# Kernel optimization log

Hardware: AMD Instinct MI355X
Metric: run time of the kernel (lower is better)

The kernel has to match this reference:

```python
import jax, jax.numpy as jnp
import numpy as np
import math

B, N, DIM = 2, 4096, 1024
H, D, M = 16, 64, 256


def setup_inputs() -> dict:
    key = jax.random.key(0)
    ks = jax.random.split(key, 6)
    s = 1.0 / math.sqrt(DIM)
    return {
        "x": jax.random.normal(ks[0], (B, N, DIM), dtype=jnp.float32),
        "w_q": jax.random.normal(ks[1], (DIM, H * D), dtype=jnp.float32) * s,
        "w_k": jax.random.normal(ks[2], (DIM, H * D), dtype=jnp.float32) * s,
        "w_v": jax.random.normal(ks[3], (DIM, H * D), dtype=jnp.float32) * s,
        "w_o": jax.random.normal(ks[4], (H * D, DIM), dtype=jnp.float32) * s,
        "b_o": jnp.zeros((DIM,), dtype=jnp.float32),
        "omega": jax.random.normal(ks[5], (M, D), dtype=jnp.float32),
    }


def _heads(t):
    # [B, N, H*D] -> [B, H, N, D]
    return t.reshape(B, N, H, D).transpose(0, 2, 1, 3)


def _phi(t, omega):
    # t: [B,H,N,D], omega: [M,D] -> [B,H,N,M]
    proj = jnp.einsum("bhnd,md->bhnm", t, omega)
    norm = 0.5 * jnp.sum(t * t, axis=-1, keepdims=True)
    return jnp.exp(proj - norm) / math.sqrt(M)


def reference(x, w_q, w_k, w_v, w_o, b_o, omega):
    q = _heads(x @ w_q)
    k = _heads(x @ w_k)
    v = _heads(x @ w_v)
    phi_q = _phi(q, omega)          # [B,H,N,M]
    phi_k = _phi(k, omega)          # [B,H,N,M]
    kv = jnp.einsum("bhnm,bhnd->bhmd", phi_k, v)   # [B,H,M,D]
    k_sum = phi_k.sum(axis=2)                       # [B,H,M]
    z = 1.0 / (jnp.einsum("bhnm,bhm->bhn", phi_q, k_sum) + 1e-6)
    out = jnp.einsum("bhnm,bhmd->bhnd", phi_q, kv) * z[..., None]
    out = out.transpose(0, 2, 1, 3).reshape(B, N, H * D)
    return out @ w_o + b_o
```

## Files before the change

### kernel.cpp

```cpp
#include <hip/hip_runtime.h>

#define DEVI __device__ __forceinline__

using f32x4 = __attribute__((ext_vector_type(4))) float;
using fvec4 = __attribute__((ext_vector_type(4))) float;
using s16x4 = __attribute__((ext_vector_type(4))) short;
using s16x8 = __attribute__((ext_vector_type(8))) short;

DEVI unsigned short f2bf_rn(float f) {
  union { float f; unsigned u; } v; v.f = f;
  unsigned r = v.u + 0x7fffu + ((v.u >> 16) & 1u);
  return (unsigned short)(r >> 16);
}
DEVI float bf2f(unsigned short h) {
  union { unsigned u; float f; } v; v.u = ((unsigned)h) << 16;
  return v.f;
}
DEVI f32x4 mfma16(s16x8 a, s16x8 b, f32x4 c) {
  return __builtin_amdgcn_mfma_f32_16x16x32_bf16(a, b, c, 0, 0, 0);
}
DEVI void gld16(const void* g, void* lds) {
  __builtin_amdgcn_global_load_lds(
      (const __attribute__((address_space(1))) unsigned int*)g,
      (__attribute__((address_space(3))) unsigned int*)lds, 16, 0, 0);
}

__global__ __launch_bounds__(256) void k_split_x(
    const float* __restrict__ X,
    unsigned short* __restrict__ XH, unsigned short* __restrict__ XL)
{
  size_t i = ((size_t)blockIdx.x * 256 + threadIdx.x) * 8;
  fvec4 a = *(const fvec4*)&X[i];
  fvec4 b = *(const fvec4*)&X[i + 4];
  s16x8 hv, lv;
#pragma unroll
  for (int j = 0; j < 4; ++j) {
    unsigned short h = f2bf_rn(a[j]);
    hv[j] = (short)h; lv[j] = (short)f2bf_rn(a[j] - bf2f(h));
  }
#pragma unroll
  for (int j = 0; j < 4; ++j) {
    unsigned short h = f2bf_rn(b[j]);
    hv[4 + j] = (short)h; lv[4 + j] = (short)f2bf_rn(b[j] - bf2f(h));
  }
  *(s16x8*)&XH[i] = hv;
  *(s16x8*)&XL[i] = lv;
}

__global__ __launch_bounds__(256) void k_prep_w(
    const float* __restrict__ wq, const float* __restrict__ wk,
    const float* __restrict__ wv, const float* __restrict__ wo,
    unsigned short* __restrict__ WTh, unsigned short* __restrict__ WOT)
{
  __shared__ float tile[64][65];
  const int z = blockIdx.z;
  const float* src = (z == 0) ? wq : (z == 1) ? wk : (z == 2) ? wv : wo;
  const int k0 = blockIdx.x * 64;
  const int n0 = blockIdx.y * 64;
  const int t = threadIdx.x;
#pragma unroll
  for (int j = 0; j < 4; ++j) {
    int r = (t >> 4) + 16 * j;
    int c = (t & 15) * 4;
    fvec4 v = *(const fvec4*)&src[(size_t)(k0 + r) * 1024 + n0 + c];
#pragma unroll
    for (int i = 0; i < 4; ++i) tile[r][c + i] = v[i];
  }
  __syncthreads();
#pragma unroll
  for (int j = 0; j < 4; ++j) {
    int n = (t >> 4) + 16 * j;
    int kc = (t & 15) * 4;
    s16x4 hv;
#pragma unroll
    for (int i = 0; i < 4; ++i) hv[i] = (short)f2bf_rn(tile[kc + i][n]);
    if (z < 3) {
      *(s16x4*)&WTh[(size_t)(z * 1024 + n0 + n) * 1024 + k0 + kc] = hv;
    } else {
      *(s16x4*)&WOT[(size_t)(n0 + n) * 1024 + k0 + kc] = hv;
    }
  }
}

__global__ __launch_bounds__(256) void k_gemm_qkv(
    const unsigned short* __restrict__ XH, const unsigned short* __restrict__ XL,
    const unsigned short* __restrict__ WTh,
    unsigned short* __restrict__ QH, unsigned short* __restrict__ QL,
    unsigned short* __restrict__ KH, unsigned short* __restrict__ KL,
    unsigned short* __restrict__ VB)
{
  __shared__ unsigned short AH[128 * 32], AL[128 * 32], BH[128 * 32];
  const int cb = blockIdx.x;
  const int rb = blockIdx.y;
  const int t = threadIdx.x;
  const int w = t >> 6, l = t & 63;
  const bool tp = (cb < 16);
  f32x4 acc[4][4];
#pragma unroll
  for (int a = 0; a < 4; ++a)
#pragma unroll
    for (int b = 0; b < 4; ++b) acc[a][b] = (f32x4)0.f;

  const int r0 = w * 32;
  const int lrow = l >> 2;
  const int lcol = (l & 3) * 8;
  const size_t gA0 = (size_t)(rb * 128 + r0 + lrow) * 1024 + lcol;
  const size_t gA1 = gA0 + (size_t)16 * 1024;
  const size_t gB0 = (size_t)(cb * 128 + r0 + lrow) * 1024 + lcol;
  const size_t gB1 = gB0 + (size_t)16 * 1024;
  unsigned short* ldsA0 = &AH[r0 * 32];
  unsigned short* ldsA1 = &AH[(r0 + 16) * 32];
  unsigned short* ldsL0 = &AL[r0 * 32];
  unsigned short* ldsL1 = &AL[(r0 + 16) * 32];
  unsigned short* ldsB0 = &BH[r0 * 32];
  unsigned short* ldsB1 = &BH[(r0 + 16) * 32];

  const int wm = (w & 1) * 64, wn = (w >> 1) * 64;
  const int lr = l & 15, ko = (l >> 4) * 8;

  for (int ks = 0; ks < 32; ++ks) {
    const int k0 = ks * 32;
    gld16(&XH[gA0 + k0], ldsA0);
    gld16(&XH[gA1 + k0], ldsA1);
    if (tp) {
      gld16(&XL[gA0 + k0], ldsL0);
      gld16(&XL[gA1 + k0], ldsL1);
    }
    gld16(&WTh[gB0 + k0], ldsB0);
    gld16(&WTh[gB1 + k0], ldsB1);
    __syncthreads();
    s16x8 ah[4], al[4], bh[4];
#pragma unroll
    for (int f = 0; f < 4; ++f) {
      ah[f] = *(const s16x8*)&AH[(wm + f * 16 + lr) * 32 + ko];
      bh[f] = *(const s16x8*)&BH[(wn + f * 16 + lr) * 32 + ko];
    }
    if (tp) {
#pragma unroll
      for (int f = 0; f < 4; ++f) al[f] = *(const s16x8*)&AL[(wm + f * 16 + lr) * 32 + ko];
    }
#pragma unroll
    for (int fa = 0; fa < 4; ++fa)
#pragma unroll
      for (int fb = 0; fb < 4; ++fb) {
        acc[fa][fb] = mfma16(ah[fa], bh[fb], acc[fa][fb]);
        if (tp) acc[fa][fb] = mfma16(al[fa], bh[fb], acc[fa][fb]);
      }
    __syncthreads();
  }
  const int lg = l >> 4;
#pragma unroll
  for (int fa = 0; fa < 4; ++fa)
#pragma unroll
    for (int r = 0; r < 4; ++r) {
      int row = rb * 128 + wm + fa * 16 + lg * 4 + r;
#pragma unroll
      for (int fb = 0; fb < 4; ++fb) {
        int col = cb * 128 + wn + fb * 16 + lr;
        float v = acc[fa][fb][r];
        unsigned short hs = f2bf_rn(v);
        if (cb < 8) {
          QH[(size_t)row * 1024 + col] = hs;
          QL[(size_t)row * 1024 + col] = f2bf_rn(v - bf2f(hs));
        } else if (cb < 16) {
          KH[(size_t)row * 1024 + col - 1024] = hs;
          KL[(size_t)row * 1024 + col - 1024] = f2bf_rn(v - bf2f(hs));
        } else {
          VB[(size_t)row * 1024 + col - 2048] = hs;
        }
      }
    }
}

__global__ __launch_bounds__(512, 1) void k_phik_kv(
    const unsigned short* __restrict__ KH, const unsigned short* __restrict__ KL,
    const unsigned short* __restrict__ VB,
    const float* __restrict__ omega, float* __restrict__ KVP)
{
  __shared__ unsigned short OH[256][72];
  __shared__ unsigned short KHs[64][72], KLs[64][72];
  __shared__ unsigned short PKT[256][72];
  __shared__ unsigned short AVT[80][72];
  __shared__ float norm_s[64];
  const int nc = blockIdx.x;
  const int bh = blockIdx.y;
  const int b = bh >> 4, h = bh & 15;
  const int t = threadIdx.x, w = t >> 6, l = t & 63;
  const int lr = l & 15, lg = l >> 4, ko8 = lg * 8;

#pragma unroll
  for (int j = 0; j < 8; ++j) {
    int e = j * 512 + t;
    int m = e >> 4, c = (e & 15) * 4;
    fvec4 v = *(const fvec4*)&omega[m * 64 + c];
    s16x4 hv;
#pragma unroll
    for (int i = 0; i < 4; ++i) hv[i] = (short)f2bf_rn(v[i]);
    *(s16x4*)&OH[m][c] = hv;
  }
  for (int e = t; e < 16 * 64; e += 512) {
    int rr = e >> 6, cc = e & 63;
    AVT[64 + rr][cc] = (rr == 0) ? (unsigned short)0x3F80 : (unsigned short)0;
  }

  f32x4 acc2[5][2];
#pragma unroll
  for (int a = 0; a < 5; ++a)
#pragma unroll
    for (int bb = 0; bb < 2; ++bb) acc2[a][bb] = (f32x4)0.f;

  for (int st = 0; st < 8; ++st) {
    const int n0 = nc * 512 + st * 64;
    __syncthreads();
    {
      int r = t >> 3, c8 = (t & 7) * 8;
      size_t o = (size_t)(b * 4096 + n0 + r) * 1024 + h * 64 + c8;
      s16x8 vh = *(const s16x8*)&KH[o];
      s16x8 vl = *(const s16x8*)&KL[o];
      *(s16x8*)&KHs[r][c8] = vh;
      *(s16x8*)&KLs[r][c8] = vl;
      float ss = 0.f;
#pragma unroll
      for (int i = 0; i < 8; ++i) {
        float q = bf2f((unsigned short)vh[i]) + bf2f((unsigned short)vl[i]);
        ss += q * q;
      }
      ss += __shfl_xor(ss, 1);
      ss += __shfl_xor(ss, 2);
      ss += __shfl_xor(ss, 4);
      if ((t & 7) == 0) norm_s[r] = 0.5f * ss;
    }
    {
      int n = t >> 3, dq = (t & 7) * 8;
      s16x8 v = *(const s16x8*)&VB[(size_t)(b * 4096 + n0 + n) * 1024 + h * 64 + dq];
#pragma unroll
      for (int i = 0; i < 8; ++i) AVT[dq + i][n] = (unsigned short)v[i];
    }
    __syncthreads();
    f32x4 acc[4][2];
#pragma unroll
    for (int a = 0; a < 4; ++a)
#pragma unroll
      for (int bb = 0; bb < 2; ++bb) acc[a][bb] = (f32x4)0.f;
#pragma unroll
    for (int ksub = 0; ksub < 2; ++ksub) {
      int ko = ksub * 32 + ko8;
      s16x8 ah[4], al[4], bh[2];
#pragma unroll
      for (int f = 0; f < 4; ++f) {
        ah[f] = *(const s16x8*)&KHs[f * 16 + lr][ko];
        al[f] = *(const s16x8*)&KLs[f * 16 + lr][ko];
      }
#pragma unroll
      for (int f = 0; f < 2; ++f) bh[f] = *(const s16x8*)&OH[w * 32 + f * 16 + lr][ko];
#pragma unroll
      for (int fa = 0; fa < 4; ++fa)
#pragma unroll
        for (int fb = 0; fb < 2; ++fb) {
          acc[fa][fb] = mfma16(ah[fa], bh[fb], acc[fa][fb]);
          acc[fa][fb] = mfma16(al[fa], bh[fb], acc[fa][fb]);
        }
    }
#pragma unroll
    for (int fa = 0; fa < 4; ++fa)
#pragma unroll
      for (int r = 0; r < 4; ++r) {
        int n = fa * 16 + lg * 4 + r;
        float nm = norm_s[n];
#pragma unroll
        for (int fb = 0; fb < 2; ++fb) {
          int m = w * 32 + fb * 16 + lr;
          float p = __expf(acc[fa][fb][r] - nm) * 0.0625f;
          PKT[m][n] = f2bf_rn(p);
        }
      }
    __syncthreads();
#pragma unroll
    for (int ksub = 0; ksub < 2; ++ksub) {
      int ko = ksub * 32 + ko8;
      s16x8 fA[5], fB[2];
#pragma unroll
      for (int f = 0; f < 5; ++f) fA[f] = *(const s16x8*)&AVT[f * 16 + lr][ko];
#pragma unroll
      for (int f = 0; f < 2; ++f) fB[f] = *(const s16x8*)&PKT[w * 32 + f * 16 + lr][ko];
#pragma unroll
      for (int fa = 0; fa < 5; ++fa)
#pragma unroll
        for (int fb = 0; fb < 2; ++fb) acc2[fa][fb] = mfma16(fA[fa], fB[fb], acc2[fa][fb]);
    }
  }
#pragma unroll
  for (int fa = 0; fa < 5; ++fa)
#pragma unroll
    for (int r = 0; r < 4; ++r) {
      int dp = fa * 16 + lg * 4 + r;
#pragma unroll
      for (int fb = 0; fb < 2; ++fb) {
        int m = w * 32 + fb * 16 + lr;
        KVP[(size_t)((bh * 8 + nc) * 80 + dp) * 256 + m] = acc2[fa][fb][r];
      }
    }
}

__global__ __launch_bounds__(256) void k_kv_reduce(
    const float* __restrict__ KVP, float* __restrict__ KVT)
{
  int idx = blockIdx.x * 256 + threadIdx.x;
  if (idx >= 32 * 80 * 256) return;
  int bh = idx / (80 * 256);
  int rem = idx % (80 * 256);
  float s = 0.f;
#pragma unroll
  for (int nci = 0; nci < 8; ++nci) s += KVP[(size_t)(bh * 8 + nci) * 80 * 256 + rem];
  KVT[idx] = s;
}

__global__ __launch_bounds__(256) void k_phiq_attn(
    const unsigned short* QH, const unsigned short* QL,
    const float* __restrict__ omega, const float* __restrict__ KVT,
    unsigned short* ATT)
{
  __shared__ unsigned short QHs[64][72], QLs[64][72];
  __shared__ unsigned short OH[256][72];
  __shared__ unsigned short PQ[64][264];
  __shared__ unsigned short KVB[80][264];
  __shared__ float norm_s[64];
  const int nt = blockIdx.x;
  const int bh = blockIdx.y;
  const int t = threadIdx.x, w = t >> 6, l = t & 63;
  const int b = bh >> 4, h = bh & 15;
  const int lr = l & 15, lg = l >> 4, ko8 = lg * 8;

  {
    int r = t >> 2, cq = (t & 3) * 4;
    float ss = 0.f;
#pragma unroll
    for (int j = 0; j < 4; ++j) {
      int c = cq + 16 * j;
      size_t o = (size_t)(b * 4096 + nt * 64 + r) * 1024 + h * 64 + c;
      s16x4 vh = *(const s16x4*)&QH[o];
      s16x4 vl = *(const s16x4*)&QL[o];
      *(s16x4*)&QHs[r][c] = vh;
      *(s16x4*)&QLs[r][c] = vl;
#pragma unroll
      for (int i = 0; i < 4; ++i) {
        float q = bf2f((unsigned short)vh[i]) + bf2f((unsigned short)vl[i]);
        ss += q * q;
      }
    }
    ss += __shfl_xor(ss, 1);
    ss += __shfl_xor(ss, 2);
    if ((t & 3) == 0) norm_s[r] = 0.5f * ss;
  }
#pragma unroll
  for (int j = 0; j < 16; ++j) {
    int e = j * 256 + t;
    int m = e >> 4, c = (e & 15) * 4;
    fvec4 v = *(const fvec4*)&omega[m * 64 + c];
    s16x4 hv;
#pragma unroll
    for (int i = 0; i < 4; ++i) hv[i] = (short)f2bf_rn(v[i]);
    *(s16x4*)&OH[m][c] = hv;
  }
#pragma unroll
  for (int j = 0; j < 20; ++j) {
    int e = (j * 256 + t) * 4;
    int dp = e >> 8, m = e & 255;
    fvec4 v = *(const fvec4*)&KVT[(size_t)bh * 80 * 256 + dp * 256 + m];
    s16x4 hv;
#pragma unroll
    for (int i = 0; i < 4; ++i) hv[i] = (short)f2bf_rn(v[i]);
    *(s16x4*)&KVB[dp][m] = hv;
  }
  __syncthreads();
  f32x4 acc[4][4];
#pragma unroll
  for (int a = 0; a < 4; ++a)
#pragma unroll
    for (int bb = 0; bb < 4; ++bb) acc[a][bb] = (f32x4)0.f;
#pragma unroll
  for (int ksub = 0; ksub < 2; ++ksub) {
    int ko = ksub * 32 + ko8;
    s16x8 ah[4], al[4], bh[4];
#pragma unroll
    for (int f = 0; f < 4; ++f) {
      ah[f] = *(const s16x8*)&QHs[f * 16 + lr][ko];
      al[f] = *(const s16x8*)&QLs[f * 16 + lr][ko];
      bh[f] = *(const s16x8*)&OH[w * 64 + f * 16 + lr][ko];
    }
#pragma unroll
    for (int fa = 0; fa < 4; ++fa)
#pragma unroll
      for (int fb = 0; fb < 4; ++fb) {
        acc[fa][fb] = mfma16(ah[fa], bh[fb], acc[fa][fb]);
        acc[fa][fb] = mfma16(al[fa], bh[fb], acc[fa][fb]);
      }
  }
#pragma unroll
  for (int fa = 0; fa < 4; ++fa)
#pragma unroll
    for (int r = 0; r < 4; ++r) {
      int n = fa * 16 + lg * 4 + r;
      float nm = norm_s[n];
#pragma unroll
      for (int fb = 0; fb < 4; ++fb) {
        int m = w * 64 + fb * 16 + lr;
        float p = __expf(acc[fa][fb][r] - nm) * 0.0625f;
        PQ[n][m] = f2bf_rn(p);
      }
    }
  __syncthreads();
  f32x4 acc2[5];
#pragma unroll
  for (int bb = 0; bb < 5; ++bb) acc2[bb] = (f32x4)0.f;
  for (int ks = 0; ks < 8; ++ks) {
    const int m0 = ks * 32;
    s16x8 fA = *(const s16x8*)&PQ[w * 16 + lr][m0 + ko8];
    s16x8 fB[5];
#pragma unroll
    for (int f = 0; f < 5; ++f) fB[f] = *(const s16x8*)&KVB[f * 16 + lr][m0 + ko8];
#pragma unroll
    for (int fb = 0; fb < 5; ++fb) acc2[fb] = mfma16(fA, fB[fb], acc2[fb]);
  }
#pragma unroll
  for (int r = 0; r < 4; ++r) {
    float den = __shfl(acc2[4][r], (l & 48));
    float z = 1.f / (den + 1e-6f);
    int n = nt * 64 + w * 16 + lg * 4 + r;
#pragma unroll
    for (int fb = 0; fb < 4; ++fb) {
      int col = h * 64 + fb * 16 + lr;
      ATT[(size_t)(b * 4096 + n) * 1024 + col] = f2bf_rn(acc2[fb][r] * z);
    }
  }
}

__global__ __launch_bounds__(256) void k_gemm_out(
    const unsigned short* __restrict__ ATT,
    const unsigned short* __restrict__ WOT,
    const float* __restrict__ b_o,
    float* __restrict__ OUT)
{
  __shared__ unsigned short As[128 * 32], Bs[128 * 32];
  const int cb = blockIdx.x;
  const int rb = blockIdx.y;
  const int t = threadIdx.x, w = t >> 6, l = t & 63;
  f32x4 acc[4][4];
#pragma unroll
  for (int a = 0; a < 4; ++a)
#pragma unroll
    for (int bb = 0; bb < 4; ++bb) acc[a][bb] = (f32x4)0.f;

  const int r0 = w * 32;
  const int lrow = l >> 2;
  const int lcol = (l & 3) * 8;
  const size_t gA0 = (size_t)(rb * 128 + r0 + lrow) * 1024 + lcol;
  const size_t gA1 = gA0 + (size_t)16 * 1024;
  const size_t gB0 = (size_t)(cb * 128 + r0 + lrow) * 1024 + lcol;
  const size_t gB1 = gB0 + (size_t)16 * 1024;
  unsigned short* ldsA0 = &As[r0 * 32];
  unsigned short* ldsA1 = &As[(r0 + 16) * 32];
  unsigned short* ldsB0 = &Bs[r0 * 32];
  unsigned short* ldsB1 = &Bs[(r0 + 16) * 32];

  const int wm = (w & 1) * 64, wn = (w >> 1) * 64;
  const int lr = l & 15, ko = (l >> 4) * 8;

  for (int ks = 0; ks < 32; ++ks) {
    const int k0 = ks * 32;
    gld16(&ATT[gA0 + k0], ldsA0);
    gld16(&ATT[gA1 + k0], ldsA1);
    gld16(&WOT[gB0 + k0], ldsB0);
    gld16(&WOT[gB1 + k0], ldsB1);
    __syncthreads();
    s16x8 fA[4], fB[4];
#pragma unroll
    for (int f = 0; f < 4; ++f) {
      fA[f] = *(const s16x8*)&As[(wm + f * 16 + lr) * 32 + ko];
      fB[f] = *(const s16x8*)&Bs[(wn + f * 16 + lr) * 32 + ko];
    }
#pragma unroll
    for (int fa = 0; fa < 4; ++fa)
#pragma unroll
      for (int fb = 0; fb < 4; ++fb) acc[fa][fb] = mfma16(fA[fa], fB[fb], acc[fa][fb]);
    __syncthreads();
  }
  const int lg = l >> 4;
#pragma unroll
  for (int fa = 0; fa < 4; ++fa)
#pragma unroll
    for (int r = 0; r < 4; ++r) {
      int row = rb * 128 + wm + fa * 16 + lg * 4 + r;
#pragma unroll
      for (int fb = 0; fb < 4; ++fb) {
        int col = cb * 128 + wn + fb * 16 + lr;
        OUT[(size_t)row * 1024 + col] = acc[fa][fb][r] + b_o[col];
      }
    }
}

extern "C" void kernel_launch(void* const* d_in, const int* in_sizes, int n_in,
                              void* d_out, int out_size, void* d_ws, size_t ws_size,
                              hipStream_t stream)
{
  const float* x  = (const float*)d_in[0];
  const float* wq = (const float*)d_in[1];
  const float* wk = (const float*)d_in[2];
  const float* wv = (const float*)d_in[3];
  const float* wo = (const float*)d_in[4];
  const float* bo = (const float*)d_in[5];
  const float* om = (const float*)d_in[6];
  float* out = (float*)d_out;

  const size_t PLANE = (size_t)8192 * 1024 * 2;
  char* ws = (char*)d_ws;
  unsigned short* WOT = (unsigned short*)(ws);
  char* segB = ws + 2097152;
  char* segC = segB + 2 * PLANE;
  char* segD = segC + 4 * PLANE;
  char* segE = segD + 26214400;

  unsigned short* QH  = (unsigned short*)segB;
  unsigned short* QL  = (unsigned short*)(segB + PLANE);
  unsigned short* ATT = (unsigned short*)segB;

  unsigned short* KH  = (unsigned short*)segC;
  unsigned short* KL  = (unsigned short*)(segC + PLANE);
  unsigned short* VB  = (unsigned short*)(segC + 2 * PLANE);
  unsigned short* XH  = (unsigned short*)(segC + 3 * PLANE);

  unsigned short* WTh = (unsigned short*)segD;
  unsigned short* XL  = (unsigned short*)(segD + 6291456);
  float* KVP = (float*)segD;
  float* KVT = (float*)segE;

  k_split_x<<<dim3(4096), 256, 0, stream>>>(x, XH, XL);
  k_prep_w<<<dim3(16, 16, 4), 256, 0, stream>>>(wq, wk, wv, wo, WTh, WOT);
  k_gemm_qkv<<<dim3(24, 64), 256, 0, stream>>>(XH, XL, WTh, QH, QL, KH, KL, VB);
  k_phik_kv<<<dim3(8, 32), 512, 0, stream>>>(KH, KL, VB, om, KVP);
  k_kv_reduce<<<dim3(2560), 256, 0, stream>>>(KVP, KVT);
  k_phiq_attn<<<dim3(64, 32), 256, 0, stream>>>(QH, QL, om, KVT, ATT);
  k_gemm_out<<<dim3(8, 64), 256, 0, stream>>>(ATT, WOT, bo, out);
}
```

Measured before the change: 233.3 us.

## Double-buffer LDS in QKV and output GEMMs and split QKV by precision

Both GEMM kernels now use two LDS buffers and prefetch the next K-slice with global_load_lds before computing the current one. Explicit vmcnt waits and raw barriers replace the two __syncthreads per iteration. The QKV GEMM becomes a template on whether the low-precision X plane is used, launched as two kernels (Q/K with hi+lo, V with hi only), which removes the per-block runtime branch and sizes LDS per variant. The cost is double the LDS footprint, which may lower occupancy, plus an extra kernel launch. The hand-counted vmcnt values must match the number of issued loads.

```diff
diff --git a/kernel.cpp b/kernel.cpp
--- a/kernel.cpp
+++ b/kernel.cpp
@@ -82,19 +82,21 @@
   }
 }
 
-__global__ __launch_bounds__(256) void k_gemm_qkv(
+template <bool TP>
+__global__ __launch_bounds__(256) void k_gemm_qkv_t(
     const unsigned short* __restrict__ XH, const unsigned short* __restrict__ XL,
-    const unsigned short* __restrict__ WTh,
+    const unsigned short* __restrict__ WTh, int cb_base,
     unsigned short* __restrict__ QH, unsigned short* __restrict__ QL,
     unsigned short* __restrict__ KH, unsigned short* __restrict__ KL,
     unsigned short* __restrict__ VB)
 {
-  __shared__ unsigned short AH[128 * 32], AL[128 * 32], BH[128 * 32];
-  const int cb = blockIdx.x;
+  __shared__ unsigned short AH[2][128 * 32];
+  __shared__ unsigned short BHs[2][128 * 32];
+  __shared__ unsigned short AL[TP ? 2 : 1][128 * 32];
+  const int cb = cb_base + blockIdx.x;
   const int rb = blockIdx.y;
   const int t = threadIdx.x;
   const int w = t >> 6, l = t & 63;
-  const bool tp = (cb < 16);
   f32x4 acc[4][4];
 #pragma unroll
   for (int a = 0; a < 4; ++a)
@@ -104,49 +106,58 @@
   const int r0 = w * 32;
   const int lrow = l >> 2;
   const int lcol = (l & 3) * 8;
-  const size_t gA0 = (size_t)(rb * 128 + r0 + lrow) * 1024 + lcol;
-  const size_t gA1 = gA0 + (size_t)16 * 1024;
-  const size_t gB0 = (size_t)(cb * 128 + r0 + lrow) * 1024 + lcol;
-  const size_t gB1 = gB0 + (size_t)16 * 1024;
-  unsigned short* ldsA0 = &AH[r0 * 32];
-  unsigned short* ldsA1 = &AH[(r0 + 16) * 32];
-  unsigned short* ldsL0 = &AL[r0 * 32];
-  unsigned short* ldsL1 = &AL[(r0 + 16) * 32];
-  unsigned short* ldsB0 = &BH[r0 * 32];
-  unsigned short* ldsB1 = &BH[(r0 + 16) * 32];
+  const size_t gA = (size_t)(rb * 128 + r0 + lrow) * 1024 + lcol;
+  const size_t gB = (size_t)(cb * 128 + r0 + lrow) * 1024 + lcol;
+  const int lds0 = r0 * 32;
+  const int lds1 = (r0 + 16) * 32;
 
   const int wm = (w & 1) * 64, wn = (w >> 1) * 64;
   const int lr = l & 15, ko = (l >> 4) * 8;
 
+  auto STAGE = [&](int buf, int k0) {
+    gld16(&XH[gA + k0], &AH[buf][lds0]);
+    gld16(&XH[gA + (size_t)16 * 1024 + k0], &AH[buf][lds1]);
+    if constexpr (TP) {
+      gld16(&XL[gA + k0], &AL[buf][lds0]);
+      gld16(&XL[gA + (size_t)16 * 1024 + k0], &AL[buf][lds1]);
+    }
+    gld16(&WTh[gB + k0], &BHs[buf][lds0]);
+    gld16(&WTh[gB + (size_t)16 * 1024 + k0], &BHs[buf][lds1]);
+  };
+
+  STAGE(0, 0);
+  int cur = 0;
   for (int ks = 0; ks < 32; ++ks) {
-    const int k0 = ks * 32;
-    gld16(&XH[gA0 + k0], ldsA0);
-    gld16(&XH[gA1 + k0], ldsA1);
-    if (tp) {
-      gld16(&XL[gA0 + k0], ldsL0);
-      gld16(&XL[gA1 + k0], ldsL1);
-    }
-    gld16(&WTh[gB0 + k0], ldsB0);
-    gld16(&WTh[gB1 + k0], ldsB1);
-    __syncthreads();
+    if (ks < 31) {
+      STAGE(cur ^ 1, (ks + 1) * 32);
+      if constexpr (TP) asm volatile("s_waitcnt vmcnt(6)" ::: "memory");
+      else              asm volatile("s_waitcnt vmcnt(4)" ::: "memory");
+    } else {
+      asm volatile("s_waitcnt vmcnt(0)" ::: "memory");
+    }
+    __builtin_amdgcn_s_barrier();
+    asm volatile("" ::: "memory");
     s16x8 ah[4], al[4], bh[4];
 #pragma unroll
     for (int f = 0; f < 4; ++f) {
-      ah[f] = *(const s16x8*)&AH[(wm + f * 16 + lr) * 32 + ko];
-      bh[f] = *(const s16x8*)&BH[(wn + f * 16 + lr) * 32 + ko];
-    }
-    if (tp) {
-#pragma unroll
-      for (int f = 0; f < 4; ++f) al[f] = *(const s16x8*)&AL[(wm + f * 16 + lr) * 32 + ko];
+      ah[f] = *(const s16x8*)&AH[cur][(wm + f * 16 + lr) * 32 + ko];
+      bh[f] = *(const s16x8*)&BHs[cur][(wn + f * 16 + lr) * 32 + ko];
+    }
+    if constexpr (TP) {
+#pragma unroll
+      for (int f = 0; f < 4; ++f) al[f] = *(const s16x8*)&AL[cur][(wm + f * 16 + lr) * 32 + ko];
     }
 #pragma unroll
     for (int fa = 0; fa < 4; ++fa)
 #pragma unroll
       for (int fb = 0; fb < 4; ++fb) {
         acc[fa][fb] = mfma16(ah[fa], bh[fb], acc[fa][fb]);
-        if (tp) acc[fa][fb] = mfma16(al[fa], bh[fb], acc[fa][fb]);
-      }
-    __syncthreads();
+        if constexpr (TP) acc[fa][fb] = mfma16(al[fa], bh[fb], acc[fa][fb]);
+      }
+    asm volatile("s_waitcnt lgkmcnt(0)" ::: "memory");
+    __builtin_amdgcn_s_barrier();
+    asm volatile("" ::: "memory");
+    cur ^= 1;
   }
   const int lg = l >> 4;
 #pragma unroll
@@ -158,15 +169,18 @@
       for (int fb = 0; fb < 4; ++fb) {
         int col = cb * 128 + wn + fb * 16 + lr;
         float v = acc[fa][fb][r];
-        unsigned short hs = f2bf_rn(v);
-        if (cb < 8) {
-          QH[(size_t)row * 1024 + col] = hs;
-          QL[(size_t)row * 1024 + col] = f2bf_rn(v - bf2f(hs));
-        } else if (cb < 16) {
-          KH[(size_t)row * 1024 + col - 1024] = hs;
-          KL[(size_t)row * 1024 + col - 1024] = f2bf_rn(v - bf2f(hs));
+        if constexpr (TP) {
+          unsigned short hs = f2bf_rn(v);
+          unsigned short ls = f2bf_rn(v - bf2f(hs));
+          if (cb < 8) {
+            QH[(size_t)row * 1024 + col] = hs;
+            QL[(size_t)row * 1024 + col] = ls;
+          } else {
+            KH[(size_t)row * 1024 + col - 1024] = hs;
+            KL[(size_t)row * 1024 + col - 1024] = ls;
+          }
         } else {
-          VB[(size_t)row * 1024 + col - 2048] = hs;
+          VB[(size_t)row * 1024 + col - 2048] = f2bf_rn(v);
         }
       }
     }
@@ -441,7 +455,7 @@
     const float* __restrict__ b_o,
     float* __restrict__ OUT)
 {
-  __shared__ unsigned short As[128 * 32], Bs[128 * 32];
+  __shared__ unsigned short As[2][128 * 32], Bs[2][128 * 32];
   const int cb = blockIdx.x;
   const int rb = blockIdx.y;
   const int t = threadIdx.x, w = t >> 6, l = t & 63;
@@ -454,36 +468,46 @@
   const int r0 = w * 32;
   const int lrow = l >> 2;
   const int lcol = (l & 3) * 8;
-  const size_t gA0 = (size_t)(rb * 128 + r0 + lrow) * 1024 + lcol;
-  const size_t gA1 = gA0 + (size_t)16 * 1024;
-  const size_t gB0 = (size_t)(cb * 128 + r0 + lrow) * 1024 + lcol;
-  const size_t gB1 = gB0 + (size_t)16 * 1024;
-  unsigned short* ldsA0 = &As[r0 * 32];
-  unsigned short* ldsA1 = &As[(r0 + 16) * 32];
-  unsigned short* ldsB0 = &Bs[r0 * 32];
-  unsigned short* ldsB1 = &Bs[(r0 + 16) * 32];
+  const size_t gA = (size_t)(rb * 128 + r0 + lrow) * 1024 + lcol;
+  const size_t gB = (size_t)(cb * 128 + r0 + lrow) * 1024 + lcol;
+  const int lds0 = r0 * 32;
+  const int lds1 = (r0 + 16) * 32;
 
   const int wm = (w & 1) * 64, wn = (w >> 1) * 64;
   const int lr = l & 15, ko = (l >> 4) * 8;
 
+  auto STAGE = [&](int buf, int k0) {
+    gld16(&ATT[gA + k0], &As[buf][lds0]);
+    gld16(&ATT[gA + (size_t)16 * 1024 + k0], &As[buf][lds1]);
+    gld16(&WOT[gB + k0], &Bs[buf][lds0]);
+    gld16(&WOT[gB + (size_t)16 * 1024 + k0], &Bs[buf][lds1]);
+  };
+
+  STAGE(0, 0);
+  int cur = 0;
   for (int ks = 0; ks < 32; ++ks) {
-    const int k0 = ks * 32;
-    gld16(&ATT[gA0 + k0], ldsA0);
-    gld16(&ATT[gA1 + k0], ldsA1);
-    gld16(&WOT[gB0 + k0], ldsB0);
-    gld16(&WOT[gB1 + k0], ldsB1);
-    __syncthreads();
+    if (ks < 31) {
+      STAGE(cur ^ 1, (ks + 1) * 32);
+      asm volatile("s_waitcnt vmcnt(4)" ::: "memory");
+    } else {
+      asm volatile("s_waitcnt vmcnt(0)" ::: "memory");
+    }
+    __builtin_amdgcn_s_barrier();
+    asm volatile("" ::: "memory");
     s16x8 fA[4], fB[4];
 #pragma unroll
     for (int f = 0; f < 4; ++f) {
-      fA[f] = *(const s16x8*)&As[(wm + f * 16 + lr) * 32 + ko];
-      fB[f] = *(const s16x8*)&Bs[(wn + f * 16 + lr) * 32 + ko];
+      fA[f] = *(const s16x8*)&As[cur][(wm + f * 16 + lr) * 32 + ko];
+      fB[f] = *(const s16x8*)&Bs[cur][(wn + f * 16 + lr) * 32 + ko];
     }
 #pragma unroll
     for (int fa = 0; fa < 4; ++fa)
 #pragma unroll
       for (int fb = 0; fb < 4; ++fb) acc[fa][fb] = mfma16(fA[fa], fB[fb], acc[fa][fb]);
-    __syncthreads();
+    asm volatile("s_waitcnt lgkmcnt(0)" ::: "memory");
+    __builtin_amdgcn_s_barrier();
+    asm volatile("" ::: "memory");
+    cur ^= 1;
   }
   const int lg = l >> 4;
 #pragma unroll
@@ -536,7 +560,8 @@
 
   k_split_x<<<dim3(4096), 256, 0, stream>>>(x, XH, XL);
   k_prep_w<<<dim3(16, 16, 4), 256, 0, stream>>>(wq, wk, wv, wo, WTh, WOT);
-  k_gemm_qkv<<<dim3(24, 64), 256, 0, stream>>>(XH, XL, WTh, QH, QL, KH, KL, VB);
+  k_gemm_qkv_t<true><<<dim3(16, 64), 256, 0, stream>>>(XH, XL, WTh, 0,  QH, QL, KH, KL, VB);
+  k_gemm_qkv_t<false><<<dim3(8, 64), 256, 0, stream>>>(XH, XL, WTh, 16, QH, QL, KH, KL, VB);
   k_phik_kv<<<dim3(8, 32), 512, 0, stream>>>(KH, KL, VB, om, KVP);
   k_kv_reduce<<<dim3(2560), 256, 0, stream>>>(KVP, KVT);
   k_phiq_attn<<<dim3(64, 32), 256, 0, stream>>>(QH, QL, om, KVT, ATT);
```

Result: slower. 264.3 us (+13.3%).
